# Performance work log

Measured on AMD Instinct MI355X. Metric: run time of the kernel, lower is better.

## Reference

```python
import jax, jax.numpy as jnp
import numpy as np

B, T, C, H, NUM_EDGE_TYPES = 2, 512, 256, 8, 16


def setup_inputs() -> dict:
    key = jax.random.key(0)
    ks = jax.random.split(key, 8)
    init = 0.02
    x = jax.random.normal(ks[0], (B, T, C), dtype=jnp.float32)
    bias_matrix = jax.random.randint(ks[1], (B, T, T), 0, NUM_EDGE_TYPES)
    w_attn = jax.random.normal(ks[2], (C, 3 * C), dtype=jnp.float32) * init
    w_proj = jax.random.normal(ks[3], (C, C), dtype=jnp.float32) * init
    w_edge_k = jax.random.normal(ks[4], (C, C), dtype=jnp.float32) * init
    w_edge_v = jax.random.normal(ks[5], (C, C), dtype=jnp.float32) * init
    edge_emb_table = jax.random.normal(ks[6], (NUM_EDGE_TYPES, C), dtype=jnp.float32)
    attn_bias_table = jax.random.normal(ks[7], (NUM_EDGE_TYPES, H), dtype=jnp.float32)
    return {
        "x": x,
        "bias_matrix": bias_matrix,
        "w_attn": w_attn,
        "w_proj": w_proj,
        "w_edge_k": w_edge_k,
        "w_edge_v": w_edge_v,
        "edge_emb_table": edge_emb_table,
        "attn_bias_table": attn_bias_table,
    }


def reference(x, bias_matrix, w_attn, w_proj, w_edge_k, w_edge_v,
              edge_emb_table, attn_bias_table):
    b, t, c = x.shape
    h = attn_bias_table.shape[1]
    e = c // h
    scale = jnp.sqrt(jnp.asarray(e, x.dtype))

    qkv = x @ w_attn                              # (B,T,3C)
    q, k, v = jnp.split(qkv, 3, axis=-1)
    # (B,H,T,E)
    q = q.reshape(b, t, h, e).transpose(0, 2, 1, 3)
    k = k.reshape(b, t, h, e).transpose(0, 2, 1, 3)
    v = v.reshape(b, t, h, e).transpose(0, 2, 1, 3)

    # edge-type embeddings and per-pair k/v modulation, (B,T,T,H,E)
    ee = edge_emb_table[bias_matrix]              # (B,T,T,C)
    e_k = (ee @ w_edge_k).reshape(b, t, t, h, e)
    e_v = (ee @ w_edge_v).reshape(b, t, t, h, e)

    # scores[b,h,i,j] = sum_e q[b,h,i,e] * k[b,h,j,e] * e_k[b, j, i, h, e]
    # (torch: e_k permuted to (B,H,j,i,E), broadcast-multiplied by k then
    #  contracted with q via 'bhie,bhjie->bhij')
    scores = jnp.einsum('bhie,bhje,bjihe->bhij', q, k, e_k) / scale

    causal = jnp.tril(jnp.ones((t, t), dtype=bool))  # (T,T)
    scores = jnp.where(causal, scores, -jnp.inf)

    # edge-type attention bias: (B,T,T,H) -> (B,H,T,T), zeroed above diagonal
    bias = attn_bias_table[bias_matrix].transpose(0, 3, 1, 2)
    bias = jnp.where(causal, bias, jnp.zeros((), bias.dtype))

    attn = jax.nn.softmax(scores + bias, axis=-1)  # (B,H,T,T)

    # y[b,h,i,e] = sum_j attn[b,h,i,j] * v[b,h,j,e] * e_v[b, j, i, h, e]
    y = jnp.einsum('bhij,bhje,bjihe->bhie', attn, v, e_v)
    y = y.transpose(0, 2, 1, 3).reshape(b, t, c)
    return y @ w_proj
```

## Files before the change

kernel.cpp:

```cpp
#include <hip/hip_runtime.h>
#include <hip/hip_bf16.h>
#include <math.h>

#define Bdim 2
#define Tdim 512
#define Cdim 256
#define Hdim 8
#define Edim 32
#define NTYPES 16
#define TI 8
#define JT 128

__global__ __launch_bounds__(256) void pre_kernel(
    const float* __restrict__ A, const float* __restrict__ Bw,
    const float* __restrict__ emb, const float* __restrict__ wk,
    const float* __restrict__ wv,
    float* __restrict__ qT, float* __restrict__ kT, float* __restrict__ vT,
    float* __restrict__ ekt, float* __restrict__ evt)
{
    __shared__ float smem[16 * 34 + 16 * 64];
    int tid = threadIdx.x;

    if (blockIdx.x >= 384) {
        int t = blockIdx.x - 384;
        float* se = smem;
        se[tid] = emb[t * Cdim + tid];
        __syncthreads();
        float a = 0.f, b = 0.f;
        for (int k = 0; k < Cdim; ++k) {
            float ev = se[k];
            a = fmaf(ev, wk[k * Cdim + tid], a);
            b = fmaf(ev, wv[k * Cdim + tid], b);
        }
        ekt[t * Cdim + tid] = a;
        evt[t * Cdim + tid] = b;
        return;
    }

    const int N = 3 * Cdim;
    const int K = Cdim;
    float (*As)[34] = (float(*)[34])smem;
    float (*Bs)[64] = (float(*)[64])(smem + 16 * 34);
    int m0 = (blockIdx.x / 12) * 32;
    int n0 = (blockIdx.x % 12) * 64;
    int tr = tid >> 4, tc = tid & 15;
    float acc[2][4] = {};
    int bkr = tid >> 4, bcq = (tid & 15) * 4;

    for (int k0 = 0; k0 < K; k0 += 16) {
        if (tid < 128) {
            int r = tid >> 2, kq = (tid & 3) * 4;
            float4 av = *(const float4*)(A + (size_t)(m0 + r) * K + k0 + kq);
            As[kq + 0][r] = av.x;
            As[kq + 1][r] = av.y;
            As[kq + 2][r] = av.z;
            As[kq + 3][r] = av.w;
        }
        float4 bv = *(const float4*)(Bw + (size_t)(k0 + bkr) * N + n0 + bcq);
        *(float4*)&Bs[bkr][bcq] = bv;
        __syncthreads();
#pragma unroll
        for (int kk = 0; kk < 16; ++kk) {
            float2 a2 = *(float2*)&As[kk][tr * 2];
            float4 b4 = *(float4*)&Bs[kk][tc * 4];
            acc[0][0] = fmaf(a2.x, b4.x, acc[0][0]);
            acc[0][1] = fmaf(a2.x, b4.y, acc[0][1]);
            acc[0][2] = fmaf(a2.x, b4.z, acc[0][2]);
            acc[0][3] = fmaf(a2.x, b4.w, acc[0][3]);
            acc[1][0] = fmaf(a2.y, b4.x, acc[1][0]);
            acc[1][1] = fmaf(a2.y, b4.y, acc[1][1]);
            acc[1][2] = fmaf(a2.y, b4.z, acc[1][2]);
            acc[1][3] = fmaf(a2.y, b4.w, acc[1][3]);
        }
        __syncthreads();
    }
    int sec = n0 >> 8;
    float* dst = (sec == 0) ? qT : (sec == 1) ? kT : vT;
    int cc0 = (n0 & 255) + tc * 4;
    int h = cc0 >> 5;
    int e0 = cc0 & 31;
#pragma unroll
    for (int i = 0; i < 2; ++i) {
        int m = m0 + tr * 2 + i;
        int bq = m >> 9, t = m & (Tdim - 1);
        float4 val = make_float4(acc[i][0], acc[i][1], acc[i][2], acc[i][3]);
        *(float4*)&dst[(((size_t)bq * Hdim + h) * Tdim + t) * Edim + e0] = val;
    }
}

__global__ __launch_bounds__(512, 4) void attn_kernel(
    const float* __restrict__ qT, const float* __restrict__ kT,
    const float* __restrict__ vT, const int* __restrict__ bm,
    const float* __restrict__ ekt, const float* __restrict__ evt,
    const float* __restrict__ abt, float* __restrict__ y)
{
    __shared__ float kv[JT][36];
    __shared__ float qm[TI][NTYPES][36];
    __shared__ float ss[TI][516];
    __shared__ unsigned int st1pf[Tdim];
    __shared__ unsigned int st2pf[Tdim];
    __shared__ float sekt[NTYPES][36];
    __shared__ float sevt[NTYPES][36];
    __shared__ float sq[TI][36];
    __shared__ float sabt[NTYPES];
    __shared__ float sinv[TI];

    float* spart = (float*)qm;

    const int pairIdx = blockIdx.x;
    const int bh = blockIdx.y;
    const int h = bh & (Hdim - 1);
    const int b = bh >> 3;
    const int tid = threadIdx.x;
    const int wave = tid >> 6;
    const int lane = tid & 63;
    const float inv_scale = 0.17677669529663687f;

    const float* qbase = qT + (size_t)bh * Tdim * Edim;
    const float* kbase = kT + (size_t)bh * Tdim * Edim;
    const float* vbase = vT + (size_t)bh * Tdim * Edim;
    const int* bmb = bm + (size_t)b * Tdim * Tdim;

    if (tid < 128) {
        int t = tid >> 3, eq = tid & 7;
        *(float4*)&sekt[t][eq * 4] = *(const float4*)&ekt[t * Cdim + h * Edim + eq * 4];
        *(float4*)&sevt[t][eq * 4] = *(const float4*)&evt[t * Cdim + h * Edim + eq * 4];
    }
    if (tid < NTYPES) sabt[tid] = abt[tid * Hdim + h];

    for (int rep = 0; rep < 2; ++rep) {
        int tau = rep ? (63 - pairIdx) : pairIdx;
        int i0 = tau * TI;
        int imax = i0 + TI - 1;
        int njt = (imax >> 7) + 1;
        int jmax = njt << 7;

        __syncthreads();

        if (tid < TI * 8) {
            int r = tid >> 3, eq = tid & 7;
            *(float4*)&sq[r][eq * 4] =
                *(const float4*)&qbase[(size_t)(i0 + r) * Edim + eq * 4];
        }
        if (tid < jmax) {
            const int* rowp = bmb + (size_t)tid * Tdim + i0;
            int4 lo = *(const int4*)rowp;
            int4 hi = *(const int4*)(rowp + 4);
            st1pf[tid] =
                ((unsigned)(lo.x & 15)) | (((unsigned)(lo.y & 15)) << 4) |
                (((unsigned)(lo.z & 15)) << 8) | (((unsigned)(lo.w & 15)) << 12) |
                (((unsigned)(hi.x & 15)) << 16) | (((unsigned)(hi.y & 15)) << 20) |
                (((unsigned)(hi.z & 15)) << 24) | (((unsigned)(hi.w & 15)) << 28);
            unsigned w2 = 0;
#pragma unroll
            for (int iiq = 0; iiq < 8; ++iiq)
                w2 |= ((unsigned)(bmb[(size_t)(i0 + iiq) * Tdim + tid] & 15)) << (iiq * 4);
            st2pf[tid] = w2;
        }
        {
            int r0 = tid >> 3, eq0 = tid & 7;
            *(float4*)&kv[r0][eq0 * 4] =
                *(const float4*)&kbase[(size_t)r0 * Edim + eq0 * 4];
            int idx1 = tid + 512;
            int r1 = idx1 >> 3, eq1 = idx1 & 7;
            *(float4*)&kv[r1][eq1 * 4] =
                *(const float4*)&kbase[(size_t)r1 * Edim + eq1 * 4];
        }
        __syncthreads();
        for (int idx = tid; idx < TI * NTYPES * 8; idx += 512) {
            int eq = idx & 7;
            int t = (idx >> 3) & (NTYPES - 1);
            int r = idx >> 7;
            float4 qv = *(float4*)&sq[r][eq * 4];
            float4 ev = *(float4*)&sekt[t][eq * 4];
            float4 o;
            o.x = qv.x * ev.x; o.y = qv.y * ev.y;
            o.z = qv.z * ev.z; o.w = qv.w * ev.w;
            *(float4*)&qm[r][t][eq * 4] = o;
        }

        for (int jt = 0; jt < njt; ++jt) {
            int j0 = jt << 7;
            if (jt > 0) {
                __syncthreads();
                for (int idx = tid; idx < JT * 8; idx += 512) {
                    int r = idx >> 3, eq = idx & 7;
                    *(float4*)&kv[r][eq * 4] =
                        *(const float4*)&kbase[(size_t)(j0 + r) * Edim + eq * 4];
                }
            }
            __syncthreads();

            int jsub = wave & 1;
            int jl = (jsub << 6) + lane;
            int j = j0 + jl;
            float4 k4[8];
#pragma unroll
            for (int eq = 0; eq < 8; ++eq) k4[eq] = *(float4*)&kv[jl][eq * 4];
            unsigned tp = st1pf[j];
            unsigned tp2 = st2pf[j];

#pragma unroll
            for (int u = 0; u < 2; ++u) {
                int ii = (wave >> 1) + (u << 2);
                int i = i0 + ii;
                if (j0 + (jsub << 6) > i) continue;
                int t1 = (tp >> (ii * 4)) & 15;
                int t2 = (tp2 >> (ii * 4)) & 15;
                float s = 0.f;
#pragma unroll
                for (int eq = 0; eq < 8; ++eq) {
                    float4 qv = *(float4*)&qm[ii][t1][eq * 4];
                    s = fmaf(qv.x, k4[eq].x, s);
                    s = fmaf(qv.y, k4[eq].y, s);
                    s = fmaf(qv.z, k4[eq].z, s);
                    s = fmaf(qv.w, k4[eq].w, s);
                }
                if (j <= i) ss[ii][j] = s * inv_scale + sabt[t2];
            }
        }
        __syncthreads();

        {
            int r0 = tid >> 3, eq0 = tid & 7;
            *(float4*)&kv[r0][eq0 * 4] =
                *(const float4*)&vbase[(size_t)r0 * Edim + eq0 * 4];
            int idx1 = tid + 512;
            int r1 = idx1 >> 3, eq1 = idx1 & 7;
            *(float4*)&kv[r1][eq1 * 4] =
                *(const float4*)&vbase[(size_t)r1 * Edim + eq1 * 4];
        }
        {
            int ii = wave;
            int i = i0 + ii;
            float m = -1e30f;
            for (int j = lane; j <= i; j += 64) m = fmaxf(m, ss[ii][j]);
            for (int off = 32; off; off >>= 1) m = fmaxf(m, __shfl_xor(m, off));
            float sum = 0.f;
            for (int j = lane; j <= i; j += 64) {
                float p = __expf(ss[ii][j] - m);
                ss[ii][j] = p;
                sum += p;
            }
            for (int off = 32; off; off >>= 1) sum += __shfl_xor(sum, off);
            if (lane == 0) sinv[ii] = 1.0f / sum;
        }

        float4 acc[TI];
#pragma unroll
        for (int ii = 0; ii < TI; ++ii) acc[ii] = make_float4(0.f, 0.f, 0.f, 0.f);
        int gid = tid >> 3;
        int eqg = tid & 7;
        for (int jt = 0; jt < njt; ++jt) {
            int j0 = jt << 7;
            if (jt > 0) {
                __syncthreads();
                for (int idx = tid; idx < JT * 8; idx += 512) {
                    int r = idx >> 3, eq = idx & 7;
                    *(float4*)&kv[r][eq * 4] =
                        *(const float4*)&vbase[(size_t)(j0 + r) * Edim + eq * 4];
                }
            }
            __syncthreads();
#pragma unroll
            for (int sub = 0; sub < 2; ++sub) {
                int jl = (sub << 6) + gid;
                int j = j0 + jl;
                float4 v4 = *(float4*)&kv[jl][eqg * 4];
                unsigned tp = st1pf[j];
#pragma unroll
                for (int ii = 0; ii < TI; ++ii) {
                    int i = i0 + ii;
                    if (j0 + (sub << 6) > i) continue;
                    float p = (j <= i) ? ss[ii][j] : 0.f;
                    int t1 = (tp >> (ii * 4)) & 15;
                    float4 ev = *(float4*)&sevt[t1][eqg * 4];
                    acc[ii].x = fmaf(p * ev.x, v4.x, acc[ii].x);
                    acc[ii].y = fmaf(p * ev.y, v4.y, acc[ii].y);
                    acc[ii].z = fmaf(p * ev.z, v4.z, acc[ii].z);
                    acc[ii].w = fmaf(p * ev.w, v4.w, acc[ii].w);
                }
            }
        }
#pragma unroll
        for (int ii = 0; ii < TI; ++ii) {
#pragma unroll
            for (int m = 8; m <= 32; m <<= 1) {
                acc[ii].x += __shfl_xor(acc[ii].x, m);
                acc[ii].y += __shfl_xor(acc[ii].y, m);
                acc[ii].z += __shfl_xor(acc[ii].z, m);
                acc[ii].w += __shfl_xor(acc[ii].w, m);
            }
        }
        if (lane < 8) {
#pragma unroll
            for (int ii = 0; ii < TI; ++ii)
                *(float4*)&spart[((wave * TI + ii) << 5) + lane * 4] = acc[ii];
        }
        __syncthreads();
        if (tid < TI * Edim) {
            int ii = tid >> 5, e = tid & 31;
            float yv = 0.f;
#pragma unroll
            for (int w = 0; w < 8; ++w) yv += spart[((w * TI + ii) << 5) + e];
            yv *= sinv[ii];
            y[((size_t)(b * Tdim + i0 + ii)) * Cdim + h * Edim + e] = yv;
        }
    }
}

__global__ __launch_bounds__(256) void proj_gemm_kernel(
    const float* __restrict__ A, const float* __restrict__ Bw,
    float* __restrict__ out)
{
    const int N = Cdim;
    const int K = Cdim;
    __shared__ float As[16][34];
    __shared__ float Bs[16][64];
    int m0 = blockIdx.y * 32;
    int n0 = blockIdx.x * 64;
    int tid = threadIdx.x;
    int tr = tid >> 4, tc = tid & 15;
    float acc[2][4] = {};
    int bkr = tid >> 4, bcq = (tid & 15) * 4;

    for (int k0 = 0; k0 < K; k0 += 16) {
        if (tid < 128) {
            int r = tid >> 2, kq = (tid & 3) * 4;
            float4 av = *(const float4*)(A + (size_t)(m0 + r) * K + k0 + kq);
            As[kq + 0][r] = av.x;
            As[kq + 1][r] = av.y;
            As[kq + 2][r] = av.z;
            As[kq + 3][r] = av.w;
        }
        float4 bv = *(const float4*)(Bw + (size_t)(k0 + bkr) * N + n0 + bcq);
        *(float4*)&Bs[bkr][bcq] = bv;
        __syncthreads();
#pragma unroll
        for (int kk = 0; kk < 16; ++kk) {
            float2 a2 = *(float2*)&As[kk][tr * 2];
            float4 b4 = *(float4*)&Bs[kk][tc * 4];
            acc[0][0] = fmaf(a2.x, b4.x, acc[0][0]);
            acc[0][1] = fmaf(a2.x, b4.y, acc[0][1]);
            acc[0][2] = fmaf(a2.x, b4.z, acc[0][2]);
            acc[0][3] = fmaf(a2.x, b4.w, acc[0][3]);
            acc[1][0] = fmaf(a2.y, b4.x, acc[1][0]);
            acc[1][1] = fmaf(a2.y, b4.y, acc[1][1]);
            acc[1][2] = fmaf(a2.y, b4.z, acc[1][2]);
            acc[1][3] = fmaf(a2.y, b4.w, acc[1][3]);
        }
        __syncthreads();
    }
#pragma unroll
    for (int i = 0; i < 2; ++i) {
        int m = m0 + tr * 2 + i;
        float4 val = make_float4(acc[i][0], acc[i][1], acc[i][2], acc[i][3]);
        *(float4*)&out[(size_t)m * N + n0 + tc * 4] = val;
    }
}

extern "C" void kernel_launch(void* const* d_in, const int* in_sizes, int n_in,
                              void* d_out, int out_size, void* d_ws, size_t ws_size,
                              hipStream_t stream) {
    (void)in_sizes; (void)n_in; (void)out_size; (void)ws_size;
    const float* x = (const float*)d_in[0];
    const int* bias_matrix = (const int*)d_in[1];
    const float* w_attn = (const float*)d_in[2];
    const float* w_proj = (const float*)d_in[3];
    const float* w_edge_k = (const float*)d_in[4];
    const float* w_edge_v = (const float*)d_in[5];
    const float* edge_emb = (const float*)d_in[6];
    const float* attn_bias = (const float*)d_in[7];
    float* out = (float*)d_out;

    const size_t n_qkv = (size_t)Bdim * Hdim * Tdim * Edim;
    float* ws = (float*)d_ws;
    float* qT = ws;
    float* kT = qT + n_qkv;
    float* vT = kT + n_qkv;
    float* y = vT + n_qkv;
    float* ekt = y + (size_t)Bdim * Tdim * Cdim;
    float* evt = ekt + (size_t)NTYPES * Cdim;

    pre_kernel<<<400, 256, 0, stream>>>(x, w_attn, edge_emb, w_edge_k, w_edge_v,
                                        qT, kT, vT, ekt, evt);
    attn_kernel<<<dim3(32, 16), 512, 0, stream>>>(qT, kT, vT, bias_matrix,
                                                  ekt, evt, attn_bias, y);
    proj_gemm_kernel<<<dim3(4, 32), 256, 0, stream>>>(y, w_proj, out);
}
```

Baseline: 132.9 us.

## Fuse score, softmax and PV per key tile with online softmax

Replaces the two-pass attention (compute all scores into a full-row shared buffer, softmax, then accumulate V) with a single pass over 128-key tiles that keeps a running max and sum and rescales accumulators. The full 8x516 score buffer and full-length type tables shrink to per-tile sizes, and launch_bounds occupancy is raised from 4 to 6 blocks. In exchange it adds extra syncthreads per tile, rescale work, and fewer registers per thread, which may cause spills.

```diff
diff --git a/kernel.cpp b/kernel.cpp
--- a/kernel.cpp
+++ b/kernel.cpp
@@ -88,7 +88,7 @@
     }
 }
 
-__global__ __launch_bounds__(512, 4) void attn_kernel(
+__global__ __launch_bounds__(512, 6) void attn_kernel(
     const float* __restrict__ qT, const float* __restrict__ kT,
     const float* __restrict__ vT, const int* __restrict__ bm,
     const float* __restrict__ ekt, const float* __restrict__ evt,
@@ -96,14 +96,14 @@
 {
     __shared__ float kv[JT][36];
     __shared__ float qm[TI][NTYPES][36];
-    __shared__ float ss[TI][516];
-    __shared__ unsigned int st1pf[Tdim];
-    __shared__ unsigned int st2pf[Tdim];
+    __shared__ float ssp[TI][132];
+    __shared__ unsigned int st1pt[JT];
+    __shared__ unsigned int st2pt[JT];
     __shared__ float sekt[NTYPES][36];
     __shared__ float sevt[NTYPES][36];
     __shared__ float sq[TI][36];
     __shared__ float sabt[NTYPES];
-    __shared__ float sinv[TI];
+    __shared__ float sm[TI], sl[TI], salpha[TI];
 
     float* spart = (float*)qm;
 
@@ -133,7 +133,6 @@
         int i0 = tau * TI;
         int imax = i0 + TI - 1;
         int njt = (imax >> 7) + 1;
-        int jmax = njt << 7;
 
         __syncthreads();
 
@@ -142,30 +141,7 @@
             *(float4*)&sq[r][eq * 4] =
                 *(const float4*)&qbase[(size_t)(i0 + r) * Edim + eq * 4];
         }
-        if (tid < jmax) {
-            const int* rowp = bmb + (size_t)tid * Tdim + i0;
-            int4 lo = *(const int4*)rowp;
-            int4 hi = *(const int4*)(rowp + 4);
-            st1pf[tid] =
-                ((unsigned)(lo.x & 15)) | (((unsigned)(lo.y & 15)) << 4) |
-                (((unsigned)(lo.z & 15)) << 8) | (((unsigned)(lo.w & 15)) << 12) |
-                (((unsigned)(hi.x & 15)) << 16) | (((unsigned)(hi.y & 15)) << 20) |
-                (((unsigned)(hi.z & 15)) << 24) | (((unsigned)(hi.w & 15)) << 28);
-            unsigned w2 = 0;
-#pragma unroll
-            for (int iiq = 0; iiq < 8; ++iiq)
-                w2 |= ((unsigned)(bmb[(size_t)(i0 + iiq) * Tdim + tid] & 15)) << (iiq * 4);
-            st2pf[tid] = w2;
-        }
-        {
-            int r0 = tid >> 3, eq0 = tid & 7;
-            *(float4*)&kv[r0][eq0 * 4] =
-                *(const float4*)&kbase[(size_t)r0 * Edim + eq0 * 4];
-            int idx1 = tid + 512;
-            int r1 = idx1 >> 3, eq1 = idx1 & 7;
-            *(float4*)&kv[r1][eq1 * 4] =
-                *(const float4*)&kbase[(size_t)r1 * Edim + eq1 * 4];
-        }
+        if (tid < TI) { sm[tid] = -1e30f; sl[tid] = 0.f; }
         __syncthreads();
         for (int idx = tid; idx < TI * NTYPES * 8; idx += 512) {
             int eq = idx & 7;
@@ -179,100 +155,119 @@
             *(float4*)&qm[r][t][eq * 4] = o;
         }
 
-        for (int jt = 0; jt < njt; ++jt) {
-            int j0 = jt << 7;
-            if (jt > 0) {
-                __syncthreads();
-                for (int idx = tid; idx < JT * 8; idx += 512) {
-                    int r = idx >> 3, eq = idx & 7;
-                    *(float4*)&kv[r][eq * 4] =
-                        *(const float4*)&kbase[(size_t)(j0 + r) * Edim + eq * 4];
-                }
-            }
-            __syncthreads();
-
-            int jsub = wave & 1;
-            int jl = (jsub << 6) + lane;
-            int j = j0 + jl;
-            float4 k4[8];
-#pragma unroll
-            for (int eq = 0; eq < 8; ++eq) k4[eq] = *(float4*)&kv[jl][eq * 4];
-            unsigned tp = st1pf[j];
-            unsigned tp2 = st2pf[j];
-
-#pragma unroll
-            for (int u = 0; u < 2; ++u) {
-                int ii = (wave >> 1) + (u << 2);
-                int i = i0 + ii;
-                if (j0 + (jsub << 6) > i) continue;
-                int t1 = (tp >> (ii * 4)) & 15;
-                int t2 = (tp2 >> (ii * 4)) & 15;
-                float s = 0.f;
-#pragma unroll
-                for (int eq = 0; eq < 8; ++eq) {
-                    float4 qv = *(float4*)&qm[ii][t1][eq * 4];
-                    s = fmaf(qv.x, k4[eq].x, s);
-                    s = fmaf(qv.y, k4[eq].y, s);
-                    s = fmaf(qv.z, k4[eq].z, s);
-                    s = fmaf(qv.w, k4[eq].w, s);
-                }
-                if (j <= i) ss[ii][j] = s * inv_scale + sabt[t2];
-            }
-        }
-        __syncthreads();
-
-        {
-            int r0 = tid >> 3, eq0 = tid & 7;
-            *(float4*)&kv[r0][eq0 * 4] =
-                *(const float4*)&vbase[(size_t)r0 * Edim + eq0 * 4];
-            int idx1 = tid + 512;
-            int r1 = idx1 >> 3, eq1 = idx1 & 7;
-            *(float4*)&kv[r1][eq1 * 4] =
-                *(const float4*)&vbase[(size_t)r1 * Edim + eq1 * 4];
-        }
-        {
-            int ii = wave;
-            int i = i0 + ii;
-            float m = -1e30f;
-            for (int j = lane; j <= i; j += 64) m = fmaxf(m, ss[ii][j]);
-            for (int off = 32; off; off >>= 1) m = fmaxf(m, __shfl_xor(m, off));
-            float sum = 0.f;
-            for (int j = lane; j <= i; j += 64) {
-                float p = __expf(ss[ii][j] - m);
-                ss[ii][j] = p;
-                sum += p;
-            }
-            for (int off = 32; off; off >>= 1) sum += __shfl_xor(sum, off);
-            if (lane == 0) sinv[ii] = 1.0f / sum;
-        }
-
         float4 acc[TI];
 #pragma unroll
         for (int ii = 0; ii < TI; ++ii) acc[ii] = make_float4(0.f, 0.f, 0.f, 0.f);
         int gid = tid >> 3;
         int eqg = tid & 7;
+
         for (int jt = 0; jt < njt; ++jt) {
             int j0 = jt << 7;
-            if (jt > 0) {
-                __syncthreads();
-                for (int idx = tid; idx < JT * 8; idx += 512) {
-                    int r = idx >> 3, eq = idx & 7;
-                    *(float4*)&kv[r][eq * 4] =
-                        *(const float4*)&vbase[(size_t)(j0 + r) * Edim + eq * 4];
+            __syncthreads();
+            {
+                int r0 = tid >> 3, eq0 = tid & 7;
+                *(float4*)&kv[r0][eq0 * 4] =
+                    *(const float4*)&kbase[(size_t)(j0 + r0) * Edim + eq0 * 4];
+                int idx1 = tid + 512;
+                int r1 = idx1 >> 3, eq1 = idx1 & 7;
+                *(float4*)&kv[r1][eq1 * 4] =
+                    *(const float4*)&kbase[(size_t)(j0 + r1) * Edim + eq1 * 4];
+            }
+            if (tid < JT) {
+                const int* rowp = bmb + (size_t)(j0 + tid) * Tdim + i0;
+                int4 lo = *(const int4*)rowp;
+                int4 hi = *(const int4*)(rowp + 4);
+                st1pt[tid] =
+                    ((unsigned)(lo.x & 15)) | (((unsigned)(lo.y & 15)) << 4) |
+                    (((unsigned)(lo.z & 15)) << 8) | (((unsigned)(lo.w & 15)) << 12) |
+                    (((unsigned)(hi.x & 15)) << 16) | (((unsigned)(hi.y & 15)) << 20) |
+                    (((unsigned)(hi.z & 15)) << 24) | (((unsigned)(hi.w & 15)) << 28);
+                unsigned w2 = 0;
+#pragma unroll
+                for (int iiq = 0; iiq < 8; ++iiq)
+                    w2 |= ((unsigned)(bmb[(size_t)(i0 + iiq) * Tdim + j0 + tid] & 15))
+                          << (iiq * 4);
+                st2pt[tid] = w2;
+            }
+            __syncthreads();
+
+            {
+                int jsub = wave & 1;
+                int jl = (jsub << 6) + lane;
+                int j = j0 + jl;
+                float4 k4[8];
+#pragma unroll
+                for (int eq = 0; eq < 8; ++eq) k4[eq] = *(float4*)&kv[jl][eq * 4];
+                unsigned tp = st1pt[jl];
+                unsigned tp2 = st2pt[jl];
+#pragma unroll
+                for (int u = 0; u < 2; ++u) {
+                    int ii = (wave >> 1) + (u << 2);
+                    int i = i0 + ii;
+                    if (j0 + (jsub << 6) > i) continue;
+                    int t1 = (tp >> (ii * 4)) & 15;
+                    int t2 = (tp2 >> (ii * 4)) & 15;
+                    float s = 0.f;
+#pragma unroll
+                    for (int eq = 0; eq < 8; ++eq) {
+                        float4 qv = *(float4*)&qm[ii][t1][eq * 4];
+                        s = fmaf(qv.x, k4[eq].x, s);
+                        s = fmaf(qv.y, k4[eq].y, s);
+                        s = fmaf(qv.z, k4[eq].z, s);
+                        s = fmaf(qv.w, k4[eq].w, s);
+                    }
+                    if (j <= i) ssp[ii][jl] = s * inv_scale + sabt[t2];
                 }
             }
             __syncthreads();
+
+            {
+                int r0 = tid >> 3, eq0 = tid & 7;
+                *(float4*)&kv[r0][eq0 * 4] =
+                    *(const float4*)&vbase[(size_t)(j0 + r0) * Edim + eq0 * 4];
+                int idx1 = tid + 512;
+                int r1 = idx1 >> 3, eq1 = idx1 & 7;
+                *(float4*)&kv[r1][eq1 * 4] =
+                    *(const float4*)&vbase[(size_t)(j0 + r1) * Edim + eq1 * 4];
+            }
+            {
+                int ii = wave;
+                int i = i0 + ii;
+                float s0 = (j0 + lane <= i) ? ssp[ii][lane] : -1e30f;
+                float s1 = (j0 + 64 + lane <= i) ? ssp[ii][64 + lane] : -1e30f;
+                float mx = fmaxf(s0, s1);
+                for (int off = 32; off; off >>= 1) mx = fmaxf(mx, __shfl_xor(mx, off));
+                float m_old = sm[ii];
+                float m_new = fmaxf(m_old, mx);
+                float p0 = __expf(s0 - m_new);
+                float p1 = __expf(s1 - m_new);
+                ssp[ii][lane] = p0;
+                ssp[ii][64 + lane] = p1;
+                float sum = p0 + p1;
+                for (int off = 32; off; off >>= 1) sum += __shfl_xor(sum, off);
+                if (lane == 0) {
+                    salpha[ii] = __expf(m_old - m_new);
+                    sm[ii] = m_new;
+                    sl[ii] = sl[ii] * salpha[ii] + sum;
+                }
+            }
+            __syncthreads();
+
+#pragma unroll
+            for (int ii = 0; ii < TI; ++ii) {
+                float a = salpha[ii];
+                acc[ii].x *= a; acc[ii].y *= a; acc[ii].z *= a; acc[ii].w *= a;
+            }
 #pragma unroll
             for (int sub = 0; sub < 2; ++sub) {
                 int jl = (sub << 6) + gid;
-                int j = j0 + jl;
                 float4 v4 = *(float4*)&kv[jl][eqg * 4];
-                unsigned tp = st1pf[j];
+                unsigned tp = st1pt[jl];
 #pragma unroll
                 for (int ii = 0; ii < TI; ++ii) {
                     int i = i0 + ii;
                     if (j0 + (sub << 6) > i) continue;
-                    float p = (j <= i) ? ss[ii][j] : 0.f;
+                    float p = ssp[ii][jl];
                     int t1 = (tp >> (ii * 4)) & 15;
                     float4 ev = *(float4*)&sevt[t1][eqg * 4];
                     acc[ii].x = fmaf(p * ev.x, v4.x, acc[ii].x);
@@ -292,6 +287,7 @@
                 acc[ii].w += __shfl_xor(acc[ii].w, m);
             }
         }
+        __syncthreads();
         if (lane < 8) {
 #pragma unroll
             for (int ii = 0; ii < TI; ++ii)
@@ -303,7 +299,7 @@
             float yv = 0.f;
 #pragma unroll
             for (int w = 0; w < 8; ++w) yv += spart[((w * TI + ii) << 5) + e];
-            yv *= sinv[ii];
+            yv /= sl[ii];
             y[((size_t)(b * Tdim + i0 + ii)) * Cdim + h * Edim + e] = yv;
         }
     }
```

Measured after the change: 230.6 us. +73.5%, slower.
